# Kernel tuning notes

Hardware: AMD Instinct MI355X
Metric: run time of the kernel (lower is better)

The kernel has to match this reference:

```python
import jax, jax.numpy as jnp
import numpy as np

N = 16384          # replayed items
D_STATE = 2048     # state_dim
D_SEM = 1024       # semantic_dim
S = 4096           # num_semantic_slots
LR = 0.01
DIST_THRESH = 2.0


def setup_inputs() -> dict:
    key = jax.random.key(0)
    k1, k2, k3 = jax.random.split(key, 3)
    replayed_states = jax.random.normal(k1, (N, D_STATE), dtype=jnp.float32)
    replayed_rewards = jax.random.normal(k2, (N,), dtype=jnp.float32)
    # small weight scale so projected content std ~0.05 -> nearest distances
    # straddle the 2.0 threshold and both branches get exercised
    W = jax.random.normal(k3, (D_SEM, D_STATE), dtype=jnp.float32) * (0.05 / np.sqrt(D_STATE))
    b = jnp.zeros((D_SEM,), dtype=jnp.float32)
    semantic_traces = jnp.zeros((S, D_SEM), dtype=jnp.float32)
    trace_strengths = jnp.zeros((S,), dtype=jnp.float32)
    return {
        "replayed_states": replayed_states,
        "replayed_rewards": replayed_rewards,
        "W": W,
        "b": b,
        "semantic_traces": semantic_traces,
        "trace_strengths": trace_strengths,
    }


def _consolidate(content_all, rewards, traces0, strengths0):
    slot_ids = jnp.arange(S, dtype=jnp.int32)

    def step(carry, xs):
        traces, strengths, ptr, num = carry
        content, reward = xs
        reward = jnp.abs(reward)
        valid = jnp.minimum(num, S)
        # euclidean distances to valid slots (invalid -> +inf)
        d = jnp.sqrt(jnp.sum((traces - content[None, :]) ** 2, axis=1))
        d = jnp.where(slot_ids < valid, d, jnp.inf)
        nearest = jnp.argmin(d).astype(jnp.int32)
        nearest_dist = d[nearest]
        do_update = (num > 0) & (nearest_dist < DIST_THRESH)

        # branch A: EMA update of nearest slot
        eff_lr = LR * (1.0 + reward)
        delta = content - traces[nearest]
        traces_u = traces.at[nearest].add(delta * eff_lr)
        strengths_u = strengths.at[nearest].add(1.0)

        # branch B: insert at ring-buffer ptr
        traces_i = traces.at[ptr].set(content)
        strengths_i = strengths.at[ptr].set(1.0)
        ptr_i = (ptr + 1) % S
        num_i = jnp.minimum(num + 1, S)

        traces_n = jnp.where(do_update, traces_u, traces_i)
        strengths_n = jnp.where(do_update, strengths_u, strengths_i)
        ptr_n = jnp.where(do_update, ptr, ptr_i)
        num_n = jnp.where(do_update, num, num_i)
        return (traces_n, strengths_n, ptr_n, num_n), None

    init = (traces0, strengths0, jnp.int32(0), jnp.int32(0))
    (traces, strengths, ptr, num), _ = jax.lax.scan(step, init, (content_all, rewards))
    return traces, strengths, num


def reference(replayed_states, replayed_rewards, W, b, semantic_traces, trace_strengths):
    # projection: nn.Linear -> x @ W.T + b
    content_all = replayed_states @ W.T + b  # (N, D_SEM)
    traces, strengths, num = _consolidate(
        content_all, replayed_rewards, semantic_traces, trace_strengths
    )
    valid_mask = (jnp.arange(S) < jnp.minimum(num, S)).astype(jnp.float32)
    denom = jnp.maximum(valid_mask.sum(), 1.0)
    mean_strength = jnp.where(num > 0, (strengths * valid_mask).sum() / denom, 0.0)
    num_consolidated = jnp.int32(N)  # every item either updates or inserts
    return traces, strengths, num, num_consolidated, mean_strength


if __name__ == "__main__":
    out = reference(**setup_inputs())
    print([getattr(o, "shape", o) for o in out])
```

## Files before the change

### kernel.cpp

```cpp
#include <hip/hip_runtime.h>
#include <cstdint>
#include <cstddef>

#define N_ITEMS 16384
#define D_STATE 2048
#define D_SEM   1024
#define S_SLOTS 4096
#define DTHRESH 2.0f

#define B_ITEMS 256
#define NBLK    (N_ITEMS / B_ITEMS)
#define CHUNK_BLKS 16
#define CHUNK_ITEMS (B_ITEMS * CHUNK_BLKS)

typedef unsigned long long u64;
typedef unsigned int u32;

__global__ __launch_bounds__(256)
void gemm_kernel(const float* __restrict__ A, const float* __restrict__ W,
                 const float* __restrict__ bias, float* __restrict__ C) {
  __shared__ float As[16][68];
  __shared__ float Bs[16][68];
  const int t = threadIdx.x;
  const int ty = t >> 4, tx = t & 15;
  const int i0 = blockIdx.x * 64, j0 = blockIdx.y * 64;
  const int lrow = t >> 2, lcol = (t & 3) << 2;
  float acc[4][4] = {{0.f}};
  const float* ap = A + (size_t)(i0 + lrow) * D_STATE + lcol;
  const float* wp = W + (size_t)(j0 + lrow) * D_STATE + lcol;
  for (int k0 = 0; k0 < D_STATE; k0 += 16) {
    float4 av = *(const float4*)(ap + k0);
    float4 wv = *(const float4*)(wp + k0);
    __syncthreads();
    As[lcol + 0][lrow] = av.x; As[lcol + 1][lrow] = av.y;
    As[lcol + 2][lrow] = av.z; As[lcol + 3][lrow] = av.w;
    Bs[lcol + 0][lrow] = wv.x; Bs[lcol + 1][lrow] = wv.y;
    Bs[lcol + 2][lrow] = wv.z; Bs[lcol + 3][lrow] = wv.w;
    __syncthreads();
#pragma unroll
    for (int kk = 0; kk < 16; kk++) {
      float a[4], b[4];
#pragma unroll
      for (int y = 0; y < 4; y++) a[y] = As[kk][ty * 4 + y];
#pragma unroll
      for (int x = 0; x < 4; x++) b[x] = Bs[kk][tx * 4 + x];
#pragma unroll
      for (int y = 0; y < 4; y++)
#pragma unroll
        for (int x = 0; x < 4; x++) acc[y][x] = fmaf(a[y], b[x], acc[y][x]);
    }
  }
#pragma unroll
  for (int y = 0; y < 4; y++)
#pragma unroll
    for (int x = 0; x < 4; x++) {
      const int col = j0 + tx * 4 + x;
      C[(size_t)(i0 + ty * 4 + y) * D_SEM + col] = acc[y][x] + bias[col];
    }
}

__global__ __launch_bounds__(256)
void gram_kernel(const float* __restrict__ Cc, float* __restrict__ G) {
  const int z = blockIdx.z;
  const float* A = Cc + (size_t)z * B_ITEMS * D_SEM;
  __shared__ float As[16][68];
  __shared__ float Bs[16][68];
  const int t = threadIdx.x;
  const int ty = t >> 4, tx = t & 15;
  const int i0 = blockIdx.x * 64, j0 = blockIdx.y * 64;
  const int lrow = t >> 2, lcol = (t & 3) << 2;
  float acc[4][4] = {{0.f}};
  const float* ap = A + (size_t)(i0 + lrow) * D_SEM + lcol;
  const float* wp = A + (size_t)(j0 + lrow) * D_SEM + lcol;
  for (int k0 = 0; k0 < D_SEM; k0 += 16) {
    float4 av = *(const float4*)(ap + k0);
    float4 wv = *(const float4*)(wp + k0);
    __syncthreads();
    As[lcol + 0][lrow] = av.x; As[lcol + 1][lrow] = av.y;
    As[lcol + 2][lrow] = av.z; As[lcol + 3][lrow] = av.w;
    Bs[lcol + 0][lrow] = wv.x; Bs[lcol + 1][lrow] = wv.y;
    Bs[lcol + 2][lrow] = wv.z; Bs[lcol + 3][lrow] = wv.w;
    __syncthreads();
#pragma unroll
    for (int kk = 0; kk < 16; kk++) {
      float a[4], b[4];
#pragma unroll
      for (int y = 0; y < 4; y++) a[y] = As[kk][ty * 4 + y];
#pragma unroll
      for (int x = 0; x < 4; x++) b[x] = Bs[kk][tx * 4 + x];
#pragma unroll
      for (int y = 0; y < 4; y++)
#pragma unroll
        for (int x = 0; x < 4; x++) acc[y][x] = fmaf(a[y], b[x], acc[y][x]);
    }
  }
  float* Gz = G + (size_t)z * B_ITEMS * B_ITEMS;
#pragma unroll
  for (int y = 0; y < 4; y++)
#pragma unroll
    for (int x = 0; x < 4; x++)
      Gz[(size_t)(i0 + ty * 4 + y) * B_ITEMS + j0 + tx * 4 + x] = acc[y][x];
}

__global__ __launch_bounds__(256)
void pgemm_kernel(const float* __restrict__ A,
                  const float* __restrict__ T,
                  float* __restrict__ P,
                  const int* __restrict__ state) {
  const int limit = min(state[0] + B_ITEMS, S_SLOTS);
  const int j0 = blockIdx.y * 64;
  const int i0 = blockIdx.x * 64;
  const int t = threadIdx.x;
  const int ty = t >> 4, tx = t & 15;
  if (j0 >= limit) {
    const float4 z = {0.f, 0.f, 0.f, 0.f};
    const int col = j0 + tx * 4;
#pragma unroll
    for (int y = 0; y < 4; y++)
      *(float4*)(P + (size_t)(i0 + ty * 4 + y) * S_SLOTS + col) = z;
    return;
  }
  __shared__ float As[16][68];
  __shared__ float Bs[16][68];
  const int lrow = t >> 2, lcol = (t & 3) << 2;
  float acc[4][4] = {{0.f}};
  const float* ap = A + (size_t)(i0 + lrow) * D_SEM + lcol;
  const float* wp = T + (size_t)(j0 + lrow) * D_SEM + lcol;
  for (int k0 = 0; k0 < D_SEM; k0 += 16) {
    float4 av = *(const float4*)(ap + k0);
    float4 wv = *(const float4*)(wp + k0);
    __syncthreads();
    As[lcol + 0][lrow] = av.x; As[lcol + 1][lrow] = av.y;
    As[lcol + 2][lrow] = av.z; As[lcol + 3][lrow] = av.w;
    Bs[lcol + 0][lrow] = wv.x; Bs[lcol + 1][lrow] = wv.y;
    Bs[lcol + 2][lrow] = wv.z; Bs[lcol + 3][lrow] = wv.w;
    __syncthreads();
#pragma unroll
    for (int kk = 0; kk < 16; kk++) {
      float a[4], b[4];
#pragma unroll
      for (int y = 0; y < 4; y++) a[y] = As[kk][ty * 4 + y];
#pragma unroll
      for (int x = 0; x < 4; x++) b[x] = Bs[kk][tx * 4 + x];
#pragma unroll
      for (int y = 0; y < 4; y++)
#pragma unroll
        for (int x = 0; x < 4; x++) acc[y][x] = fmaf(a[y], b[x], acc[y][x]);
    }
  }
#pragma unroll
  for (int y = 0; y < 4; y++)
#pragma unroll
    for (int x = 0; x < 4; x++)
      P[(size_t)(i0 + ty * 4 + y) * S_SLOTS + j0 + tx * 4 + x] = acc[y][x];
}

__global__ __launch_bounds__(256)
void init_kernel(const float* __restrict__ traces0, float* __restrict__ out,
                 float* __restrict__ n_g, int* __restrict__ state) {
  __shared__ float wsum[4];
  const int s = blockIdx.x, t = threadIdx.x;
  const int lane = t & 63, wave = t >> 6;
  float4 v = *(const float4*)(traces0 + (size_t)s * D_SEM + 4 * t);
  *(float4*)(out + (size_t)s * D_SEM + 4 * t) = v;
  float nn = v.x * v.x + v.y * v.y + v.z * v.z + v.w * v.w;
#pragma unroll
  for (int o = 32; o; o >>= 1) nn += __shfl_down(nn, o, 64);
  if (lane == 0) wsum[wave] = nn;
  __syncthreads();
  if (t == 0) n_g[s] = wsum[0] + wsum[1] + wsum[2] + wsum[3];
  if (s == 0 && t == 0) { state[0] = 0; state[1] = 0; }
}

__global__ __launch_bounds__(256)
void scan_kernel(float* __restrict__ P, const float* __restrict__ Gb,
                 const float* __restrict__ rewards, const float* __restrict__ n_g,
                 int* __restrict__ state, u64* __restrict__ decs) {
  __shared__ u64 partials[2][4];
  const int t = threadIdx.x;
  const int lane = t & 63, wave = t >> 6;
  const int s_base = t << 4;

  int num = state[0];
  int ptr = state[1];

  float n_reg[16];
#pragma unroll
  for (int k = 0; k < 16; k += 4) {
    float4 nv = *(const float4*)(n_g + s_base + k);
    n_reg[k + 0] = (s_base + k + 0 < num) ? nv.x : __uint_as_float(0x7F800000u);
    n_reg[k + 1] = (s_base + k + 1 < num) ? nv.y : __uint_as_float(0x7F800000u);
    n_reg[k + 2] = (s_base + k + 2 < num) ? nv.z : __uint_as_float(0x7F800000u);
    n_reg[k + 3] = (s_base + k + 3 < num) ? nv.w : __uint_as_float(0x7F800000u);
  }

  float p_cur[16], p_nxt[16];
#pragma unroll
  for (int k = 0; k < 16; k += 4) {
    float4 v = *(const float4*)(P + s_base + k);
    p_cur[k] = v.x; p_cur[k + 1] = v.y; p_cur[k + 2] = v.z; p_cur[k + 3] = v.w;
  }
#pragma unroll
  for (int k = 0; k < 16; k++) p_nxt[k] = 0.f;

  float greg = Gb[t];
  float gi   = Gb[0];
  float ri   = rewards[0];

  u32 my_slot = 0; float my_lr = 0.f;

  for (int i = 0; i < B_ITEMS; i++) {
    float gi_n = 0.f, ri_n = 0.f, gnext = 0.f, greg_n = 0.f;
    if (i + 1 < B_ITEMS) {
      gi_n   = Gb[(size_t)(i + 1) * B_ITEMS + (i + 1)];
      ri_n   = rewards[i + 1];
      gnext  = Gb[(size_t)i * B_ITEMS + (i + 1)];
      greg_n = Gb[(size_t)(i + 1) * B_ITEMS + t];
#pragma unroll
      for (int k = 0; k < 16; k += 4) {
        float4 v = *(const float4*)(P + (size_t)(i + 1) * S_SLOTS + s_base + k);
        p_nxt[k] = v.x; p_nxt[k + 1] = v.y; p_nxt[k + 2] = v.z; p_nxt[k + 3] = v.w;
      }
    }

    u64 best = ~0ull;
#pragma unroll
    for (int k = 0; k < 16; k++) {
      const float d2 = fmaxf(fmaf(-2.0f, p_cur[k], n_reg[k] + gi), 0.f);
      const u64 key = ((u64)__float_as_uint(d2) << 32) | (u32)(s_base + k);
      if (key < best) best = key;
    }
#pragma unroll
    for (int o = 32; o; o >>= 1) {
      const u64 v = __shfl_down(best, o, 64);
      if (v < best) best = v;
    }
    if (lane == 0) partials[i & 1][wave] = best;
    __syncthreads();

    u64 bk = partials[i & 1][0];
    { u64 v = partials[i & 1][1]; if (v < bk) bk = v;
      v = partials[i & 1][2]; if (v < bk) bk = v;
      v = partials[i & 1][3]; if (v < bk) bk = v; }
    const float d2b = __uint_as_float((u32)(bk >> 32));
    const int nslot = (int)(u32)bk;
    const bool upd = (num > 0) && (sqrtf(d2b) < DTHRESH);
    const float lr = __fmul_rn(0.01f, __fadd_rn(1.0f, fabsf(ri)));
    const int slot = upd ? nslot : ptr;
    const float omr = 1.0f - lr;
    if (!upd) { num = min(num + 1, S_SLOTS); ptr = (ptr + 1) & (S_SLOTS - 1); }
    if (i == t) { my_slot = (u32)slot | (upd ? 0x80000000u : 0u); my_lr = lr; }

    if ((slot >> 4) == t) {
#define OWNFIX(K) { const float nold = n_reg[K]; float pn = p_nxt[K]; float nnew; \
      if (upd) { const float pc = 0.5f * (nold + gi - d2b); \
        nnew = omr * omr * nold + 2.0f * lr * omr * pc + lr * lr * gi; \
        pn = fmaf(omr, pn, lr * gnext); } \
      else { nnew = gi; pn = gnext; } \
      n_reg[K] = nnew; p_nxt[K] = pn; }
      switch (slot & 15) {
        case 0:  OWNFIX(0)  break; case 1:  OWNFIX(1)  break;
        case 2:  OWNFIX(2)  break; case 3:  OWNFIX(3)  break;
        case 4:  OWNFIX(4)  break; case 5:  OWNFIX(5)  break;
        case 6:  OWNFIX(6)  break; case 7:  OWNFIX(7)  break;
        case 8:  OWNFIX(8)  break; case 9:  OWNFIX(9)  break;
        case 10: OWNFIX(10) break; case 11: OWNFIX(11) break;
        case 12: OWNFIX(12) break; case 13: OWNFIX(13) break;
        case 14: OWNFIX(14) break; default: OWNFIX(15) break;
      }
#undef OWNFIX
    }

    if (t >= i + 2) {
      float* qp = P + (size_t)t * S_SLOTS + slot;
      if (upd) *qp = fmaf(omr, *qp, __fmul_rn(lr, greg));
      else     *qp = greg;
    }

#pragma unroll
    for (int k = 0; k < 16; k++) p_cur[k] = p_nxt[k];
    gi = gi_n; ri = ri_n; greg = greg_n;
    __syncthreads();
  }

  if (t == 0) { state[0] = num; state[1] = ptr; }
  decs[t] = ((u64)__float_as_uint(my_lr) << 32) | (u64)my_slot;
}

__global__ __launch_bounds__(256)
void apply_kernel(const float* __restrict__ content,
                  const u64* __restrict__ decs,
                  float* __restrict__ traces,
                  float* __restrict__ n_g) {
  __shared__ u32 aslot[B_ITEMS];
  __shared__ float alr[B_ITEMS];
  __shared__ float betas[B_ITEMS];
  __shared__ int notowner;
  __shared__ float wsum[4];
  const int t = threadIdx.x, j = blockIdx.x;
  const int lane = t & 63, wave = t >> 6;
  const u64 d = decs[t];
  aslot[t] = (u32)(d & 0xFFFFFFFFull);
  alr[t] = __uint_as_float((u32)(d >> 32));
  if (t == 0) notowner = 0;
  __syncthreads();
  const u32 myslot = aslot[j] & 0x7FFFFFFFu;
  if (t > j && (aslot[t] & 0x7FFFFFFFu) == myslot) notowner = 1;
  __syncthreads();
  if (notowner) return;

  float alpha = 1.f, beta = 0.f;
  for (int k = 0; k < B_ITEMS; k++) {
    const u32 a = aslot[k];
    if ((a & 0x7FFFFFFFu) == myslot) {
      const float lr = alr[k];
      if (a & 0x80000000u) {
        const float om = 1.f - lr;
        alpha *= om; beta *= om;
        if (t == k) beta += lr;
      } else {
        alpha = 0.f; beta = (t == k) ? 1.f : 0.f;
      }
    }
  }
  betas[t] = beta;
  __syncthreads();

  float4 v = *(const float4*)(traces + (size_t)myslot * D_SEM + 4 * t);
  v.x *= alpha; v.y *= alpha; v.z *= alpha; v.w *= alpha;
  for (int k = 0; k < B_ITEMS; k++) {
    if ((aslot[k] & 0x7FFFFFFFu) == myslot) {
      const float bk = betas[k];
      const float4 c = *(const float4*)(content + (size_t)k * D_SEM + 4 * t);
      v.x = fmaf(bk, c.x, v.x); v.y = fmaf(bk, c.y, v.y);
      v.z = fmaf(bk, c.z, v.z); v.w = fmaf(bk, c.w, v.w);
    }
  }
  *(float4*)(traces + (size_t)myslot * D_SEM + 4 * t) = v;
  float nn = v.x * v.x + v.y * v.y + v.z * v.z + v.w * v.w;
#pragma unroll
  for (int o = 32; o; o >>= 1) nn += __shfl_down(nn, o, 64);
  if (lane == 0) wsum[wave] = nn;
  __syncthreads();
  if (t == 0) n_g[myslot] = wsum[0] + wsum[1] + wsum[2] + wsum[3];
}

__global__ __launch_bounds__(256)
void finalize_kernel(const float* __restrict__ strengths0,
                     const u64* __restrict__ decs,
                     const int* __restrict__ state, float* __restrict__ out) {
  __shared__ int last_ins[S_SLOTS];
  __shared__ int cnt[S_SLOTS];
  __shared__ float wsum[4];
  const int t = threadIdx.x, lane = t & 63, wave = t >> 6;
  for (int s = t; s < S_SLOTS; s += 256) { last_ins[s] = -1; cnt[s] = 0; }
  __syncthreads();
  for (int k = t; k < N_ITEMS; k += 256) {
    const u32 dd = (u32)(decs[k] & 0xFFFFFFFFull);
    if (!(dd & 0x80000000u)) atomicMax(&last_ins[(int)dd], k);
  }
  __syncthreads();
  for (int k = t; k < N_ITEMS; k += 256) {
    const u32 dd = (u32)(decs[k] & 0xFFFFFFFFull);
    const int slot = (int)(dd & 0x7FFFFFFFu);
    if ((dd & 0x80000000u) && k > last_ins[slot]) atomicAdd(&cnt[slot], 1);
  }
  __syncthreads();
  const int num = state[0];
  float* outs = out + (size_t)S_SLOTS * D_SEM;
  float lsum = 0.f;
  for (int s = t; s < S_SLOTS; s += 256) {
    const float base = (last_ins[s] >= 0) ? 1.f : strengths0[s];
    const float v = base + (float)cnt[s];
    outs[s] = v;
    if (s < num) lsum += v;
  }
#pragma unroll
  for (int o = 32; o; o >>= 1) lsum += __shfl_down(lsum, o, 64);
  if (lane == 0) wsum[wave] = lsum;
  __syncthreads();
  if (t == 0) {
    const float total = wsum[0] + wsum[1] + wsum[2] + wsum[3];
    float denom = (float)num;
    if (denom < 1.f) denom = 1.f;
    outs[S_SLOTS + 0] = (float)num;
    outs[S_SLOTS + 1] = (float)N_ITEMS;
    outs[S_SLOTS + 2] = (num > 0) ? (total / denom) : 0.f;
  }
}

extern "C" void kernel_launch(void* const* d_in, const int* in_sizes, int n_in,
                              void* d_out, int out_size, void* d_ws, size_t ws_size,
                              hipStream_t stream) {
  const float* states  = (const float*)d_in[0];
  const float* rewards = (const float*)d_in[1];
  const float* W       = (const float*)d_in[2];
  const float* bias    = (const float*)d_in[3];
  const float* traces0 = (const float*)d_in[4];
  const float* str0    = (const float*)d_in[5];
  float* out = (float*)d_out;

  char* p = (char*)d_ws;
  float* cbuf = (float*)p;                 p += (size_t)CHUNK_ITEMS * D_SEM * 4;
  float* P    = (float*)p;                 p += (size_t)B_ITEMS * S_SLOTS * 4;
  float* Gb   = (float*)p;                 p += (size_t)CHUNK_BLKS * B_ITEMS * B_ITEMS * 4;
  float* n_g  = (float*)p;                 p += (size_t)S_SLOTS * 4;
  u64*   decs = (u64*)p;                   p += (size_t)N_ITEMS * 8;
  int*   state = (int*)p;

  init_kernel<<<S_SLOTS, 256, 0, stream>>>(traces0, out, n_g, state);

  for (int c = 0; c < N_ITEMS / CHUNK_ITEMS; c++) {
    gemm_kernel<<<dim3(CHUNK_ITEMS / 64, D_SEM / 64), 256, 0, stream>>>(
        states + (size_t)c * CHUNK_ITEMS * D_STATE, W, bias, cbuf);
    gram_kernel<<<dim3(4, 4, CHUNK_BLKS), 256, 0, stream>>>(cbuf, Gb);
    for (int bb = 0; bb < CHUNK_BLKS; bb++) {
      const int b = c * CHUNK_BLKS + bb;
      const float* cblk = cbuf + (size_t)bb * B_ITEMS * D_SEM;
      const float* Gblk = Gb + (size_t)bb * B_ITEMS * B_ITEMS;
      pgemm_kernel<<<dim3(4, S_SLOTS / 64), 256, 0, stream>>>(cblk, out, P, state);
      scan_kernel<<<1, 256, 0, stream>>>(P, Gblk, rewards + (size_t)b * B_ITEMS,
                                         n_g, state, decs + (size_t)b * B_ITEMS);
      apply_kernel<<<B_ITEMS, 256, 0, stream>>>(cblk, decs + (size_t)b * B_ITEMS,
                                                out, n_g);
    }
  }
  finalize_kernel<<<1, 256, 0, stream>>>(str0, decs, state, out);
}
```

Baseline: 34.58 ms.

## Deepen per-item scan pipeline to prefetch two rows and defer global RMW

Restructures the sequential per-block decision loop so the projection row for item i+2 is prefetched one iteration earlier, with register-level fixups applied for the two most recent decisions. The global read-modify-write of P for the previous decision is deferred by one iteration so its load latency overlaps the argmin reduction. The first barrier is also replaced by an explicit LDS wait plus s_barrier that does not drain outstanding global loads. This aims to hide global memory latency on the serial critical path, at the cost of more registers and more complex correctness bookkeeping.

```diff
diff --git a/kernel.cpp b/kernel.cpp
--- a/kernel.cpp
+++ b/kernel.cpp
@@ -194,34 +194,50 @@
     n_reg[k + 3] = (s_base + k + 3 < num) ? nv.w : __uint_as_float(0x7F800000u);
   }
 
-  float p_cur[16], p_nxt[16];
+  float p_cur[16], p_n1[16];
 #pragma unroll
   for (int k = 0; k < 16; k += 4) {
-    float4 v = *(const float4*)(P + s_base + k);
-    p_cur[k] = v.x; p_cur[k + 1] = v.y; p_cur[k + 2] = v.z; p_cur[k + 3] = v.w;
-  }
-#pragma unroll
-  for (int k = 0; k < 16; k++) p_nxt[k] = 0.f;
-
-  float greg = Gb[t];
-  float gi   = Gb[0];
-  float ri   = rewards[0];
+    float4 v0 = *(const float4*)(P + s_base + k);
+    float4 v1 = *(const float4*)(P + (size_t)S_SLOTS + s_base + k);
+    p_cur[k] = v0.x; p_cur[k + 1] = v0.y; p_cur[k + 2] = v0.z; p_cur[k + 3] = v0.w;
+    p_n1[k]  = v1.x; p_n1[k + 1]  = v1.y; p_n1[k + 2]  = v1.z; p_n1[k + 3]  = v1.w;
+  }
+
+  float gi = Gb[0];
+  float ri = rewards[0];
+
+  int  prev_slot = 0;
+  bool prev_upd = false;
+  float prev_lr = 0.f, prev_omr = 1.f;
+  float greg_prev = 0.f;
 
   u32 my_slot = 0; float my_lr = 0.f;
 
   for (int i = 0; i < B_ITEMS; i++) {
-    float gi_n = 0.f, ri_n = 0.f, gnext = 0.f, greg_n = 0.f;
+    float p_in[16] = {0.f};
+    if (i + 2 < B_ITEMS) {
+      const float* rp = P + (size_t)(i + 2) * S_SLOTS + s_base;
+#pragma unroll
+      for (int k = 0; k < 16; k += 4) {
+        float4 v = *(const float4*)(rp + k);
+        p_in[k] = v.x; p_in[k + 1] = v.y; p_in[k + 2] = v.z; p_in[k + 3] = v.w;
+      }
+    }
+    float gi_n = 0.f, ri_n = 0.f, g_ip1 = 0.f, g_ip2 = 0.f, g_prev_ip2 = 0.f;
+    float greg_i = 0.f;
     if (i + 1 < B_ITEMS) {
-      gi_n   = Gb[(size_t)(i + 1) * B_ITEMS + (i + 1)];
-      ri_n   = rewards[i + 1];
-      gnext  = Gb[(size_t)i * B_ITEMS + (i + 1)];
-      greg_n = Gb[(size_t)(i + 1) * B_ITEMS + t];
-#pragma unroll
-      for (int k = 0; k < 16; k += 4) {
-        float4 v = *(const float4*)(P + (size_t)(i + 1) * S_SLOTS + s_base + k);
-        p_nxt[k] = v.x; p_nxt[k + 1] = v.y; p_nxt[k + 2] = v.z; p_nxt[k + 3] = v.w;
-      }
-    }
+      gi_n  = Gb[(size_t)(i + 1) * B_ITEMS + (i + 1)];
+      ri_n  = rewards[i + 1];
+      g_ip1 = Gb[(size_t)i * B_ITEMS + (i + 1)];
+      greg_i = Gb[(size_t)i * B_ITEMS + t];
+    }
+    if (i + 2 < B_ITEMS) {
+      g_ip2 = Gb[(size_t)i * B_ITEMS + (i + 2)];
+      if (i >= 1) g_prev_ip2 = Gb[(size_t)(i - 1) * B_ITEMS + (i + 2)];
+    }
+    const bool do_rmw = (i >= 1) && (t >= i + 3);
+    float rmw_old = 0.f;
+    if (do_rmw && prev_upd) rmw_old = P[(size_t)t * S_SLOTS + prev_slot];
 
     u64 best = ~0ull;
 #pragma unroll
@@ -236,7 +252,9 @@
       if (v < best) best = v;
     }
     if (lane == 0) partials[i & 1][wave] = best;
-    __syncthreads();
+    asm volatile("s_waitcnt lgkmcnt(0)" ::: "memory");
+    __builtin_amdgcn_s_barrier();
+    asm volatile("" ::: "memory");
 
     u64 bk = partials[i & 1][0];
     { u64 v = partials[i & 1][1]; if (v < bk) bk = v;
@@ -251,35 +269,55 @@
     if (!upd) { num = min(num + 1, S_SLOTS); ptr = (ptr + 1) & (S_SLOTS - 1); }
     if (i == t) { my_slot = (u32)slot | (upd ? 0x80000000u : 0u); my_lr = lr; }
 
+    if (do_rmw) {
+      P[(size_t)t * S_SLOTS + prev_slot] =
+          prev_upd ? fmaf(prev_omr, rmw_old, __fmul_rn(prev_lr, greg_prev))
+                   : greg_prev;
+    }
+
+    if (i >= 1 && i + 2 < B_ITEMS && (prev_slot >> 4) == t) {
+#define ENT(K) { p_in[K] = prev_upd ? fmaf(prev_omr, p_in[K], __fmul_rn(prev_lr, g_prev_ip2)) : g_prev_ip2; }
+      switch (prev_slot & 15) {
+        case 0:  ENT(0)  break; case 1:  ENT(1)  break;
+        case 2:  ENT(2)  break; case 3:  ENT(3)  break;
+        case 4:  ENT(4)  break; case 5:  ENT(5)  break;
+        case 6:  ENT(6)  break; case 7:  ENT(7)  break;
+        case 8:  ENT(8)  break; case 9:  ENT(9)  break;
+        case 10: ENT(10) break; case 11: ENT(11) break;
+        case 12: ENT(12) break; case 13: ENT(13) break;
+        case 14: ENT(14) break; default: ENT(15) break;
+      }
+#undef ENT
+    }
+
     if ((slot >> 4) == t) {
-#define OWNFIX(K) { const float nold = n_reg[K]; float pn = p_nxt[K]; float nnew; \
+#define WFIX(K) { const float nold = n_reg[K]; float nnew; \
       if (upd) { const float pc = 0.5f * (nold + gi - d2b); \
         nnew = omr * omr * nold + 2.0f * lr * omr * pc + lr * lr * gi; \
-        pn = fmaf(omr, pn, lr * gnext); } \
-      else { nnew = gi; pn = gnext; } \
-      n_reg[K] = nnew; p_nxt[K] = pn; }
+        if (i + 1 < B_ITEMS) p_n1[K] = fmaf(omr, p_n1[K], __fmul_rn(lr, g_ip1)); \
+        if (i + 2 < B_ITEMS) p_in[K] = fmaf(omr, p_in[K], __fmul_rn(lr, g_ip2)); \
+      } else { nnew = gi; \
+        if (i + 1 < B_ITEMS) p_n1[K] = g_ip1; \
+        if (i + 2 < B_ITEMS) p_in[K] = g_ip2; } \
+      n_reg[K] = nnew; }
       switch (slot & 15) {
-        case 0:  OWNFIX(0)  break; case 1:  OWNFIX(1)  break;
-        case 2:  OWNFIX(2)  break; case 3:  OWNFIX(3)  break;
-        case 4:  OWNFIX(4)  break; case 5:  OWNFIX(5)  break;
-        case 6:  OWNFIX(6)  break; case 7:  OWNFIX(7)  break;
-        case 8:  OWNFIX(8)  break; case 9:  OWNFIX(9)  break;
-        case 10: OWNFIX(10) break; case 11: OWNFIX(11) break;
-        case 12: OWNFIX(12) break; case 13: OWNFIX(13) break;
-        case 14: OWNFIX(14) break; default: OWNFIX(15) break;
+        case 0:  WFIX(0)  break; case 1:  WFIX(1)  break;
+        case 2:  WFIX(2)  break; case 3:  WFIX(3)  break;
+        case 4:  WFIX(4)  break; case 5:  WFIX(5)  break;
+        case 6:  WFIX(6)  break; case 7:  WFIX(7)  break;
+        case 8:  WFIX(8)  break; case 9:  WFIX(9)  break;
+        case 10: WFIX(10) break; case 11: WFIX(11) break;
+        case 12: WFIX(12) break; case 13: WFIX(13) break;
+        case 14: WFIX(14) break; default: WFIX(15) break;
       }
-#undef OWNFIX
-    }
-
-    if (t >= i + 2) {
-      float* qp = P + (size_t)t * S_SLOTS + slot;
-      if (upd) *qp = fmaf(omr, *qp, __fmul_rn(lr, greg));
-      else     *qp = greg;
-    }
-
-#pragma unroll
-    for (int k = 0; k < 16; k++) p_cur[k] = p_nxt[k];
-    gi = gi_n; ri = ri_n; greg = greg_n;
+#undef WFIX
+    }
+
+#pragma unroll
+    for (int k = 0; k < 16; k++) { p_cur[k] = p_n1[k]; p_n1[k] = p_in[k]; }
+    gi = gi_n; ri = ri_n;
+    prev_slot = slot; prev_upd = upd; prev_lr = lr; prev_omr = omr;
+    greg_prev = greg_i;
     __syncthreads();
   }
 
```

Measured after the change: 36.06 ms. +4.3%, slower.

## Replace global P row writes with LDS correction buffer and deeper prefetch

Applied to the files above, without the earlier changes.

The scan kernel no longer writes back updated dot products into global P for later items. It keeps per-slot decay factors and an LDS correction buffer, which items fill via atomics and which are then applied when the next rows load. Rows are prefetched three steps ahead with double-buffered registers, and barriers become raw s_barrier calls with explicit waitcnt. The aim is to take global read-modify-write latency off the serial critical path, at the cost of more registers, an extra barrier per step, and LDS atomics.

```diff
diff --git a/kernel.cpp b/kernel.cpp
--- a/kernel.cpp
+++ b/kernel.cpp
@@ -172,17 +172,20 @@
   if (s == 0 && t == 0) { state[0] = 0; state[1] = 0; }
 }
 
-__global__ __launch_bounds__(256)
-void scan_kernel(float* __restrict__ P, const float* __restrict__ Gb,
+__global__ __launch_bounds__(256, 1)
+void scan_kernel(const float* __restrict__ P, const float* __restrict__ Gb,
                  const float* __restrict__ rewards, const float* __restrict__ n_g,
                  int* __restrict__ state, u64* __restrict__ decs) {
-  __shared__ u64 partials[2][4];
+  __shared__ float corr_buf[S_SLOTS];
+  __shared__ u64 partials[4];
   const int t = threadIdx.x;
   const int lane = t & 63, wave = t >> 6;
   const int s_base = t << 4;
 
   int num = state[0];
   int ptr = state[1];
+
+  for (int s = t; s < S_SLOTS; s += 256) corr_buf[s] = 0.f;
 
   float n_reg[16];
 #pragma unroll
@@ -193,95 +196,145 @@
     n_reg[k + 2] = (s_base + k + 2 < num) ? nv.z : __uint_as_float(0x7F800000u);
     n_reg[k + 3] = (s_base + k + 3 < num) ? nv.w : __uint_as_float(0x7F800000u);
   }
-
-  float p_cur[16], p_nxt[16];
+  float alpha_r[16];
+#pragma unroll
+  for (int k = 0; k < 16; k++) alpha_r[k] = 1.f;
+
+  float p_cur[16], p_n1[16], p_in[16];
 #pragma unroll
   for (int k = 0; k < 16; k += 4) {
-    float4 v = *(const float4*)(P + s_base + k);
-    p_cur[k] = v.x; p_cur[k + 1] = v.y; p_cur[k + 2] = v.z; p_cur[k + 3] = v.w;
-  }
-#pragma unroll
-  for (int k = 0; k < 16; k++) p_nxt[k] = 0.f;
-
-  float greg = Gb[t];
-  float gi   = Gb[0];
-  float ri   = rewards[0];
-
+    float4 v0 = *(const float4*)(P + s_base + k);
+    float4 v1 = *(const float4*)(P + (size_t)S_SLOTS + s_base + k);
+    p_cur[k] = v0.x; p_cur[k + 1] = v0.y; p_cur[k + 2] = v0.z; p_cur[k + 3] = v0.w;
+    p_n1[k]  = v1.x; p_n1[k + 1]  = v1.y; p_n1[k + 2]  = v1.z; p_n1[k + 3]  = v1.w;
+  }
+#pragma unroll
+  for (int k = 0; k < 16; k++) p_in[k] = 0.f;
+
+  float p_raw_a[16], p_raw_b[16];
+  float gc_a, gc_b;
+  {
+    const float* rp = P + (size_t)2 * S_SLOTS + s_base;
+#pragma unroll
+    for (int k = 0; k < 16; k += 4) {
+      float4 v = *(const float4*)(rp + k);
+      p_raw_a[k] = v.x; p_raw_a[k + 1] = v.y; p_raw_a[k + 2] = v.z; p_raw_a[k + 3] = v.w;
+    }
+    gc_a = Gb[(size_t)2 * B_ITEMS + t];
+    gc_b = 0.f;
+#pragma unroll
+    for (int k = 0; k < 16; k++) p_raw_b[k] = 0.f;
+  }
+
+  float gi = Gb[0];
+  float ri = rewards[0];
+  float g1 = Gb[1];
+
+  int my_cslot = -1; float my_coeff = 0.f;
   u32 my_slot = 0; float my_lr = 0.f;
 
-  for (int i = 0; i < B_ITEMS; i++) {
-    float gi_n = 0.f, ri_n = 0.f, gnext = 0.f, greg_n = 0.f;
-    if (i + 1 < B_ITEMS) {
-      gi_n   = Gb[(size_t)(i + 1) * B_ITEMS + (i + 1)];
-      ri_n   = rewards[i + 1];
-      gnext  = Gb[(size_t)i * B_ITEMS + (i + 1)];
-      greg_n = Gb[(size_t)(i + 1) * B_ITEMS + t];
-#pragma unroll
-      for (int k = 0; k < 16; k += 4) {
-        float4 v = *(const float4*)(P + (size_t)(i + 1) * S_SLOTS + s_base + k);
-        p_nxt[k] = v.x; p_nxt[k + 1] = v.y; p_nxt[k + 2] = v.z; p_nxt[k + 3] = v.w;
-      }
-    }
-
-    u64 best = ~0ull;
-#pragma unroll
-    for (int k = 0; k < 16; k++) {
-      const float d2 = fmaxf(fmaf(-2.0f, p_cur[k], n_reg[k] + gi), 0.f);
-      const u64 key = ((u64)__float_as_uint(d2) << 32) | (u32)(s_base + k);
-      if (key < best) best = key;
-    }
-#pragma unroll
-    for (int o = 32; o; o >>= 1) {
-      const u64 v = __shfl_down(best, o, 64);
-      if (v < best) best = v;
-    }
-    if (lane == 0) partials[i & 1][wave] = best;
-    __syncthreads();
-
-    u64 bk = partials[i & 1][0];
-    { u64 v = partials[i & 1][1]; if (v < bk) bk = v;
-      v = partials[i & 1][2]; if (v < bk) bk = v;
-      v = partials[i & 1][3]; if (v < bk) bk = v; }
-    const float d2b = __uint_as_float((u32)(bk >> 32));
-    const int nslot = (int)(u32)bk;
-    const bool upd = (num > 0) && (sqrtf(d2b) < DTHRESH);
-    const float lr = __fmul_rn(0.01f, __fadd_rn(1.0f, fabsf(ri)));
-    const int slot = upd ? nslot : ptr;
-    const float omr = 1.0f - lr;
-    if (!upd) { num = min(num + 1, S_SLOTS); ptr = (ptr + 1) & (S_SLOTS - 1); }
-    if (i == t) { my_slot = (u32)slot | (upd ? 0x80000000u : 0u); my_lr = lr; }
-
-    if ((slot >> 4) == t) {
-#define OWNFIX(K) { const float nold = n_reg[K]; float pn = p_nxt[K]; float nnew; \
-      if (upd) { const float pc = 0.5f * (nold + gi - d2b); \
-        nnew = omr * omr * nold + 2.0f * lr * omr * pc + lr * lr * gi; \
-        pn = fmaf(omr, pn, lr * gnext); } \
-      else { nnew = gi; pn = gnext; } \
-      n_reg[K] = nnew; p_nxt[K] = pn; }
-      switch (slot & 15) {
-        case 0:  OWNFIX(0)  break; case 1:  OWNFIX(1)  break;
-        case 2:  OWNFIX(2)  break; case 3:  OWNFIX(3)  break;
-        case 4:  OWNFIX(4)  break; case 5:  OWNFIX(5)  break;
-        case 6:  OWNFIX(6)  break; case 7:  OWNFIX(7)  break;
-        case 8:  OWNFIX(8)  break; case 9:  OWNFIX(9)  break;
-        case 10: OWNFIX(10) break; case 11: OWNFIX(11) break;
-        case 12: OWNFIX(12) break; case 13: OWNFIX(13) break;
-        case 14: OWNFIX(14) break; default: OWNFIX(15) break;
-      }
+  __syncthreads();
+
+#define OWNFIX(K, I) { const float nold = n_reg[K]; \
+    if (upd) { const float pc = 0.5f * (nold + gi - d2b); \
+      n_reg[K] = omr * omr * nold + 2.0f * lr * omr * pc + lr * lr * gi; \
+      alpha_r[K] = __fmul_rn(alpha_r[K], omr); \
+      if ((I) + 1 < B_ITEMS) p_n1[K] = fmaf(omr, p_n1[K], __fmul_rn(lr, g1)); \
+    } else { n_reg[K] = gi; alpha_r[K] = 0.f; \
+      if ((I) + 1 < B_ITEMS) p_n1[K] = g1; } }
+
+#define SCAN_STEP(I, RAWC, GCC, RAWN, GCN) { \
+     \
+    if ((I) + 3 < B_ITEMS) { \
+      const float* rp = P + (size_t)((I) + 3) * S_SLOTS + s_base; \
+      _Pragma("unroll") \
+      for (int k = 0; k < 16; k += 4) { \
+        float4 v = *(const float4*)(rp + k); \
+        RAWN[k] = v.x; RAWN[k + 1] = v.y; RAWN[k + 2] = v.z; RAWN[k + 3] = v.w; \
+      } \
+      GCN = Gb[(size_t)((I) + 3) * B_ITEMS + t]; \
+    } \
+    float gi_n = 0.f, ri_n = 0.f, g1_n = 0.f; \
+    if ((I) + 1 < B_ITEMS) { \
+      gi_n = Gb[(size_t)((I) + 1) * B_ITEMS + (I) + 1]; \
+      ri_n = rewards[(I) + 1]; \
+      if ((I) + 2 < B_ITEMS) g1_n = Gb[(size_t)((I) + 1) * B_ITEMS + (I) + 2]; \
+    } \
+     \
+    u64 best = ~0ull; \
+    _Pragma("unroll") \
+    for (int k = 0; k < 16; k++) { \
+      const float d2 = fmaxf(fmaf(-2.0f, p_cur[k], n_reg[k] + gi), 0.f); \
+      const u64 key = ((u64)__float_as_uint(d2) << 32) | (u32)(s_base + k); \
+      if (key < best) best = key; \
+    } \
+    _Pragma("unroll") \
+    for (int o = 32; o; o >>= 1) { \
+      const u64 v = __shfl_down(best, o, 64); \
+      if (v < best) best = v; \
+    } \
+    if (lane == 0) partials[wave] = best; \
+    asm volatile("s_waitcnt lgkmcnt(0)" ::: "memory"); \
+    __builtin_amdgcn_s_barrier(); \
+    __builtin_amdgcn_sched_barrier(0); \
+     \
+    u64 bk = partials[0]; \
+    { u64 v = partials[1]; if (v < bk) bk = v; \
+      v = partials[2]; if (v < bk) bk = v; \
+      v = partials[3]; if (v < bk) bk = v; } \
+    const float d2b = __uint_as_float((u32)(bk >> 32)); \
+    const int nslot = (int)(u32)bk; \
+    const bool upd = (num > 0) && (d2b < 4.0f); \
+    const float lr = __fmul_rn(0.01f, __fadd_rn(1.0f, fabsf(ri))); \
+    const int slot = upd ? nslot : ptr; \
+    const float omr = 1.0f - lr; \
+    if (!upd) { num = min(num + 1, S_SLOTS); ptr = (ptr + 1) & (S_SLOTS - 1); } \
+    if ((I) == t) { my_slot = (u32)slot | (upd ? 0x80000000u : 0u); my_lr = lr; } \
+    if (my_cslot == slot) my_coeff = upd ? __fmul_rn(my_coeff, omr) : 0.f; \
+    if ((I) == t) { my_cslot = slot; my_coeff = upd ? lr : 1.f; } \
+    if ((slot >> 4) == t) { \
+      switch (slot & 15) { \
+        case 0:  OWNFIX(0,  I) break; case 1:  OWNFIX(1,  I) break; \
+        case 2:  OWNFIX(2,  I) break; case 3:  OWNFIX(3,  I) break; \
+        case 4:  OWNFIX(4,  I) break; case 5:  OWNFIX(5,  I) break; \
+        case 6:  OWNFIX(6,  I) break; case 7:  OWNFIX(7,  I) break; \
+        case 8:  OWNFIX(8,  I) break; case 9:  OWNFIX(9,  I) break; \
+        case 10: OWNFIX(10, I) break; case 11: OWNFIX(11, I) break; \
+        case 12: OWNFIX(12, I) break; case 13: OWNFIX(13, I) break; \
+        case 14: OWNFIX(14, I) break; default: OWNFIX(15, I) break; \
+      } \
+    } \
+     \
+    if ((I) + 2 < B_ITEMS && my_coeff != 0.f) \
+      atomicAdd(&corr_buf[my_cslot], __fmul_rn(my_coeff, GCC)); \
+    asm volatile("s_waitcnt lgkmcnt(0)" ::: "memory"); \
+    __builtin_amdgcn_s_barrier(); \
+    __builtin_amdgcn_sched_barrier(0); \
+     \
+    if ((I) + 2 < B_ITEMS) { \
+      const float4 z4 = {0.f, 0.f, 0.f, 0.f}; \
+      _Pragma("unroll") \
+      for (int k = 0; k < 16; k += 4) { \
+        float4 cv = *(const float4*)(&corr_buf[s_base + k]); \
+        p_in[k + 0] = fmaf(alpha_r[k + 0], RAWC[k + 0], cv.x); \
+        p_in[k + 1] = fmaf(alpha_r[k + 1], RAWC[k + 1], cv.y); \
+        p_in[k + 2] = fmaf(alpha_r[k + 2], RAWC[k + 2], cv.z); \
+        p_in[k + 3] = fmaf(alpha_r[k + 3], RAWC[k + 3], cv.w); \
+        *(float4*)(&corr_buf[s_base + k]) = z4; \
+      } \
+    } \
+     \
+    _Pragma("unroll") \
+    for (int k = 0; k < 16; k++) { p_cur[k] = p_n1[k]; p_n1[k] = p_in[k]; } \
+    gi = gi_n; ri = ri_n; g1 = g1_n; \
+  }
+
+  for (int i = 0; i < B_ITEMS; i += 2) {
+    SCAN_STEP(i,     p_raw_a, gc_a, p_raw_b, gc_b)
+    SCAN_STEP(i + 1, p_raw_b, gc_b, p_raw_a, gc_a)
+  }
+#undef SCAN_STEP
 #undef OWNFIX
-    }
-
-    if (t >= i + 2) {
-      float* qp = P + (size_t)t * S_SLOTS + slot;
-      if (upd) *qp = fmaf(omr, *qp, __fmul_rn(lr, greg));
-      else     *qp = greg;
-    }
-
-#pragma unroll
-    for (int k = 0; k < 16; k++) p_cur[k] = p_nxt[k];
-    gi = gi_n; ri = ri_n; greg = greg_n;
-    __syncthreads();
-  }
 
   if (t == 0) { state[0] = num; state[1] = ptr; }
   decs[t] = ((u64)__float_as_uint(my_lr) << 32) | (u64)my_slot;
```

New measurement: 35.84 ms. 3.6% more time.
